# Performance work log

Hardware: AMD Instinct MI355X
Metric: run time of the kernel (lower is better)

The kernel has to match this reference:

```python
import jax, jax.numpy as jnp
import numpy as np

B, S, N, P = 16, 1, 6, 70000
H0, W0, DS = 448, 800, 4
H, W = H0 // DS, W0 // DS          # 112, 200
BEV_SIDE = 200


def _apply_4x4(RT, xyz):
    # RT: [M,4,4], xyz: [M,P,3] -> [M,P,3]
    xyz1 = jnp.concatenate([xyz, jnp.ones_like(xyz[..., :1])], axis=-1)
    return jnp.einsum('mij,mpj->mpi', RT, xyz1)[..., :3]


def _scale_intrinsics4(K, sx, sy):
    # K: [M,3,3] pinhole intrinsics -> scaled, embedded in 4x4
    M = K.shape[0]
    K4 = jnp.tile(jnp.eye(4, dtype=K.dtype), (M, 1, 1))
    K4 = K4.at[:, 0, 0].set(K[:, 0, 0] * sx)
    K4 = K4.at[:, 1, 1].set(K[:, 1, 1] * sy)
    K4 = K4.at[:, 0, 2].set(K[:, 0, 2] * sx)
    K4 = K4.at[:, 1, 2].set(K[:, 1, 2] * sy)
    return K4


def setup_inputs() -> dict:
    rng = np.random.default_rng(0)
    pts = rng.uniform(-50.0, 50.0, size=(B, 1, 1, P, 3)).astype(np.float32)
    pts[..., 2] = rng.uniform(-2.0, 4.0, size=(B, 1, 1, P)).astype(np.float32)
    ilu = rng.uniform(0.0, 255.0, size=(B, 1, 1, P, 1)).astype(np.float32)
    pcloud = np.concatenate([pts, ilu], axis=-1)
    # extrinsics: cam-to-car pose, 6 cameras at yaw 0..300deg
    E = np.tile(np.eye(4, dtype=np.float32), (B, S, N, 1, 1))
    for n in range(N):
        a = 2.0 * np.pi * n / N
        c, s = np.cos(a), np.sin(a)
        E[:, :, n, :3, :3] = np.array([[c, -s, 0], [s, c, 0], [0, 0, 1]], np.float32)
        E[:, :, n, :3, 3] = np.array([2.0 * c, 2.0 * s, 1.5], np.float32)
    K = np.tile(np.eye(3, dtype=np.float32), (B, S, N, 1, 1))
    K[..., 0, 0] = 500.0
    K[..., 1, 1] = 500.0
    K[..., 0, 2] = W0 / 2.0
    K[..., 1, 2] = H0 / 2.0
    V = np.tile(np.eye(4, dtype=np.float32), (B, 1, 1, 1, 1))
    V[..., 0, 0] = 2.0
    V[..., 1, 1] = 2.0
    V[..., 0, 3] = 100.0
    V[..., 1, 3] = 100.0
    return {
        'pcloud': jnp.asarray(pcloud),
        'extrinsics': jnp.asarray(E),
        'intrinsics': jnp.asarray(K),
        'view': jnp.asarray(V),
        'bev_side': BEV_SIDE,
    }


def reference(pcloud, extrinsics, intrinsics, view, bev_side):
    sx = sy = 1.0 / DS
    bsn = B * S * N
    lidar_coords = pcloud[:, 0, 0, :, :3]                      # [B,P,3]
    ilu = jnp.repeat(pcloud[:, 0, 0, :, 3], N, axis=0)         # [BSN,P]
    view2 = view[:, 0, 0]                                      # [B,4,4]
    lidar_view = _apply_4x4(jnp.linalg.inv(view2), lidar_coords)
    xyz_car = jnp.repeat(lidar_view, N, axis=0)                # [BSN,P,3]
    K = intrinsics.reshape(bsn, 3, 3)
    E = extrinsics.reshape(bsn, 4, 4)
    Rt = jnp.swapaxes(E[:, :3, :3], 1, 2)
    Einv = E.at[:, :3, :3].set(Rt).at[:, :3, 3:4].set(-jnp.matmul(Rt, E[:, :3, 3:4]))
    pixel_from_car = jnp.matmul(_scale_intrinsics4(K, sx, sy), Einv)
    z = _apply_4x4(Einv, xyz_car)[:, :, 2]                     # cam-frame depth
    xyz_pixel = _apply_4x4(pixel_from_car, xyz_car)            # [BSN,P,3]
    normalizer = xyz_pixel[:, :, 2]
    xy = xyz_pixel[:, :, :2] / jnp.maximum(normalizer[..., None], 1e-6)
    x_, y_ = xy[:, :, 0], xy[:, :, 1]
    valid = ((x_ > -0.5) & (x_ < W - 0.5) & (y_ > -0.5) & (y_ < H - 0.5) & (z > 0.0)).astype(pcloud.dtype)
    depth = jnp.clip(normalizer, 0.0, bev_side / 2 - 1) * valid
    vilu = jnp.clip(ilu * valid, 0.0, 255.0)
    ym = jnp.clip(y_, 0.0, H - 1).astype(jnp.int32)
    xm = jnp.clip(x_, 0.0, W - 1).astype(jnp.int32)
    b = jnp.broadcast_to(jnp.arange(bsn)[:, None], (bsn, P))
    depth_grid = jnp.zeros((bsn, H, W), pcloud.dtype).at[b, ym, xm].set(depth)
    ilu_grid = jnp.zeros((bsn, H, W), pcloud.dtype).at[b, ym, xm].set(vilu)
    ilu_grid = jnp.log1p(ilu_grid) / np.log(256.0)
    depth_grid = depth_grid / (bev_side / 2)
    return jnp.concatenate([depth_grid[:, None], ilu_grid[:, None]], axis=1)  # [BSN,2,H,W]
```

## Files before the change

kernel.cpp:

```cpp
#include <hip/hip_runtime.h>
#include <math.h>

#define B_    16
#define N_    6
#define P_    70000
#define H_    112
#define W_    200
#define HW_   (H_ * W_)
#define BSN_  (B_ * N_)
#define HALF_ 56
#define CELLS_ (HALF_ * W_)
#define THREADS_ 1024


__device__ __forceinline__ float rdot(const float r[4], float x, float y, float z) {
    float s = r[0] * x;
    s = fmaf(r[1], y, s);
    s = fmaf(r[2], z, s);
    s = s + r[3];
    return s;
}

__device__ __forceinline__ void inv4(const float* m, float* o) {
    float inv[16];
    inv[0]  =  m[5]*m[10]*m[15] - m[5]*m[11]*m[14] - m[9]*m[6]*m[15] + m[9]*m[7]*m[14] + m[13]*m[6]*m[11] - m[13]*m[7]*m[10];
    inv[4]  = -m[4]*m[10]*m[15] + m[4]*m[11]*m[14] + m[8]*m[6]*m[15] - m[8]*m[7]*m[14] - m[12]*m[6]*m[11] + m[12]*m[7]*m[10];
    inv[8]  =  m[4]*m[9]*m[15]  - m[4]*m[11]*m[13] - m[8]*m[5]*m[15] + m[8]*m[7]*m[13] + m[12]*m[5]*m[11] - m[12]*m[7]*m[9];
    inv[12] = -m[4]*m[9]*m[14]  + m[4]*m[10]*m[13] + m[8]*m[5]*m[14] - m[8]*m[6]*m[13] - m[12]*m[5]*m[10] + m[12]*m[6]*m[9];
    inv[1]  = -m[1]*m[10]*m[15] + m[1]*m[11]*m[14] + m[9]*m[2]*m[15] - m[9]*m[3]*m[14] - m[13]*m[2]*m[11] + m[13]*m[3]*m[10];
    inv[5]  =  m[0]*m[10]*m[15] - m[0]*m[11]*m[14] - m[8]*m[2]*m[15] + m[8]*m[3]*m[14] + m[12]*m[2]*m[11] - m[12]*m[3]*m[10];
    inv[9]  = -m[0]*m[9]*m[15]  + m[0]*m[11]*m[13] + m[8]*m[1]*m[15] - m[8]*m[3]*m[13] - m[12]*m[1]*m[11] + m[12]*m[3]*m[9];
    inv[13] =  m[0]*m[9]*m[14]  - m[0]*m[10]*m[13] - m[8]*m[1]*m[14] + m[8]*m[2]*m[13] + m[12]*m[1]*m[10] - m[12]*m[2]*m[9];
    inv[2]  =  m[1]*m[6]*m[15]  - m[1]*m[7]*m[14]  - m[5]*m[2]*m[15] + m[5]*m[3]*m[14] + m[13]*m[2]*m[7]  - m[13]*m[3]*m[6];
    inv[6]  = -m[0]*m[6]*m[15]  + m[0]*m[7]*m[14]  + m[4]*m[2]*m[15] - m[4]*m[3]*m[14] - m[12]*m[2]*m[7]  + m[12]*m[3]*m[6];
    inv[10] =  m[0]*m[5]*m[15]  - m[0]*m[7]*m[13]  - m[4]*m[1]*m[15] + m[4]*m[3]*m[13] + m[12]*m[1]*m[7]  - m[12]*m[3]*m[5];
    inv[14] = -m[0]*m[5]*m[14]  + m[0]*m[6]*m[13]  + m[4]*m[1]*m[14] - m[4]*m[2]*m[13] - m[12]*m[1]*m[6]  + m[12]*m[2]*m[5];
    inv[3]  = -m[1]*m[6]*m[11]  + m[1]*m[7]*m[10]  + m[5]*m[2]*m[11] - m[5]*m[3]*m[10] - m[9]*m[2]*m[7]   + m[9]*m[3]*m[6];
    inv[7]  =  m[0]*m[6]*m[11]  - m[0]*m[7]*m[10]  - m[4]*m[2]*m[11] + m[4]*m[3]*m[10] + m[8]*m[2]*m[7]   - m[8]*m[3]*m[6];
    inv[11] = -m[0]*m[5]*m[11]  + m[0]*m[7]*m[9]   + m[4]*m[1]*m[11] - m[4]*m[3]*m[9]  - m[8]*m[1]*m[7]   + m[8]*m[3]*m[5];
    inv[15] =  m[0]*m[5]*m[10]  - m[0]*m[6]*m[9]   - m[4]*m[1]*m[10] + m[4]*m[2]*m[9]  + m[8]*m[1]*m[6]   - m[8]*m[2]*m[5];
    float det = m[0]*inv[0] + m[1]*inv[4] + m[2]*inv[8] + m[3]*inv[12];
    float rdet = 1.0f / det;
    for (int i = 0; i < 16; ++i) o[i] = inv[i] * rdet;
}

__device__ __forceinline__ void cam_mats(const float* Ein, const float* Kin,
                                         float E2[4], float PFC[3][4]) {
    float Einv[4][4];
    for (int i = 0; i < 3; ++i)
        for (int j = 0; j < 3; ++j)
            Einv[i][j] = Ein[j * 4 + i];
    for (int i = 0; i < 3; ++i) {
        float s = Ein[0 * 4 + i] * Ein[0 * 4 + 3];
        s = fmaf(Ein[1 * 4 + i], Ein[1 * 4 + 3], s);
        s = fmaf(Ein[2 * 4 + i], Ein[2 * 4 + 3], s);
        Einv[i][3] = -s;
    }
    Einv[3][0] = Ein[12]; Einv[3][1] = Ein[13];
    Einv[3][2] = Ein[14]; Einv[3][3] = Ein[15];

    float K4[4][4] = {};
    K4[0][0] = Kin[0] * 0.25f;  K4[0][2] = Kin[2] * 0.25f;
    K4[1][1] = Kin[4] * 0.25f;  K4[1][2] = Kin[5] * 0.25f;
    K4[2][2] = 1.0f;            K4[3][3] = 1.0f;

    for (int i = 0; i < 3; ++i)
        for (int j = 0; j < 4; ++j) {
            float s = K4[i][0] * Einv[0][j];
            s = fmaf(K4[i][1], Einv[1][j], s);
            s = fmaf(K4[i][2], Einv[2][j], s);
            s = fmaf(K4[i][3], Einv[3][j], s);
            PFC[i][j] = s;
        }
    for (int j = 0; j < 4; ++j) E2[j] = Einv[2][j];
}


__global__ __launch_bounds__(THREADS_) void k_lidar_fused(
        const float4* __restrict__ pc, const float* __restrict__ extr,
        const float* __restrict__ intr, const float* __restrict__ view,
        float* __restrict__ out, const int* __restrict__ bev_side_p) {
    __shared__ int   win[CELLS_];
    __shared__ float sV[4][4];
    __shared__ float sE2[4];
    __shared__ float sP[3][4];

    const int i    = blockIdx.x;
    const int xcd  = i & 7;
    const int s    = i >> 3;
    const int b    = xcd + 8 * (s >= 12 ? 1 : 0);
    const int c12  = s % 12;
    const int m    = b * N_ + (c12 >> 1);
    const int rlo  = (c12 & 1) * HALF_;
    const int t    = threadIdx.x;

    if (t == 0) {
        float Vi[16];
        inv4(&view[b * 16], Vi);
        for (int ii = 0; ii < 4; ++ii)
            for (int j = 0; j < 4; ++j) sV[ii][j] = Vi[ii * 4 + j];
    } else if (t == 64) {
        float E2[4], PFC[3][4];
        cam_mats(&extr[m * 16], &intr[m * 9], E2, PFC);
        for (int j = 0; j < 4; ++j) sE2[j] = E2[j];
        for (int ii = 0; ii < 3; ++ii)
            for (int j = 0; j < 4; ++j) sP[ii][j] = PFC[ii][j];
    }
    for (int k = t; k < CELLS_; k += THREADS_) win[k] = -1;
    __syncthreads();

    const float4* pcb = pc + (size_t)b * P_;
    int c0 = -1, c1 = -1, c2 = -1, c3 = -1;
    for (int p = t; p < P_; p += THREADS_) {
        float4 pt = pcb[p];
        float lx = rdot(sV[0], pt.x, pt.y, pt.z);
        float ly = rdot(sV[1], pt.x, pt.y, pt.z);
        float lz = rdot(sV[2], pt.x, pt.y, pt.z);
        float px = rdot(sP[0], lx, ly, lz);
        float py = rdot(sP[1], lx, ly, lz);
        float pz = rdot(sP[2], lx, ly, lz);
        float denom = fmaxf(pz, 1e-6f);
        float x_ = px / denom;
        float y_ = py / denom;
        int ym = (int)fminf(fmaxf(y_, 0.0f), (float)(H_ - 1));
        int xm = (int)fminf(fmaxf(x_, 0.0f), (float)(W_ - 1));
        bool is_c = (xm == 0 || xm == W_ - 1) && (ym == 0 || ym == H_ - 1);
        int code = ((ym != 0) << 1) | (xm != 0);
        c0 = (is_c && code == 0) ? p : c0;
        c1 = (is_c && code == 1) ? p : c1;
        c2 = (is_c && code == 2) ? p : c2;
        c3 = (is_c && code == 3) ? p : c3;
        int rr = ym - rlo;
        if (!is_c && (unsigned)rr < (unsigned)HALF_)
            atomicMax(&win[rr * W_ + xm], p);
    }
    for (int d = 32; d; d >>= 1) {
        c0 = max(c0, __shfl_xor(c0, d));
        c1 = max(c1, __shfl_xor(c1, d));
        c2 = max(c2, __shfl_xor(c2, d));
        c3 = max(c3, __shfl_xor(c3, d));
    }
    if ((t & 63) == 0) {
        if (rlo == 0) {
            if (c0 >= 0) atomicMax(&win[0 * W_ + 0],        c0);
            if (c1 >= 0) atomicMax(&win[0 * W_ + (W_ - 1)], c1);
        } else {
            if (c2 >= 0) atomicMax(&win[(H_ - 1 - rlo) * W_ + 0],        c2);
            if (c3 >= 0) atomicMax(&win[(H_ - 1 - rlo) * W_ + (W_ - 1)], c3);
        }
    }
    __syncthreads();

    const float bev_half = (float)bev_side_p[0] * 0.5f;
    const float clip_hi  = bev_half - 1.0f;
    const int base0 = (m * 2) * HW_ + rlo * W_;
    for (int r = t; r < CELLS_; r += THREADS_) {
        int w = win[r];
        float depth = 0.0f, iluv = 0.0f;
        if (w >= 0) {
            float4 pt = pcb[w];
            float lx = rdot(sV[0], pt.x, pt.y, pt.z);
            float ly = rdot(sV[1], pt.x, pt.y, pt.z);
            float lz = rdot(sV[2], pt.x, pt.y, pt.z);
            float z  = rdot(sE2,   lx, ly, lz);
            float px = rdot(sP[0], lx, ly, lz);
            float py = rdot(sP[1], lx, ly, lz);
            float pz = rdot(sP[2], lx, ly, lz);
            float denom = fmaxf(pz, 1e-6f);
            float x_ = px / denom;
            float y_ = py / denom;
            bool valid = (x_ > -0.5f) && (x_ < (float)W_ - 0.5f) &&
                         (y_ > -0.5f) && (y_ < (float)H_ - 0.5f) && (z > 0.0f);
            if (valid) {
                float d = fminf(fmaxf(pz, 0.0f), clip_hi);
                depth = d / bev_half;
                float vi = fminf(fmaxf(pt.w, 0.0f), 255.0f);
                iluv = log1pf(vi) / 5.545177444479562f;
            }
        }
        out[base0 + r]       = depth;
        out[base0 + HW_ + r] = iluv;
    }
}


extern "C" void kernel_launch(void* const* d_in, const int* in_sizes, int n_in,
                              void* d_out, int out_size, void* d_ws, size_t ws_size,
                              hipStream_t stream) {
    const float4* pc  = (const float4*)d_in[0];
    const float* extr = (const float*)d_in[1];
    const float* intr = (const float*)d_in[2];
    const float* view = (const float*)d_in[3];
    const int*   bev  = (const int*)d_in[4];
    float* out = (float*)d_out;

    k_lidar_fused<<<dim3(BSN_ * 2), dim3(THREADS_), 0, stream>>>(
        pc, extr, intr, view, out, bev);
}
```

Before: 48.98 us.

## Precompute view-inverse transform in separate pass into workspace

```diff
diff --git a/kernel.cpp b/kernel.cpp
--- a/kernel.cpp
+++ b/kernel.cpp
@@ -19,6 +19,14 @@
     s = fmaf(r[2], z, s);
     s = s + r[3];
     return s;
+}
+
+__device__ __forceinline__ float rdot4(float r0, float r1, float r2, float r3,
+                                       float x, float y, float z) {
+    float s = r0 * x;
+    s = fmaf(r1, y, s);
+    s = fmaf(r2, z, s);
+    return s + r3;
 }
 
 __device__ __forceinline__ void inv4(const float* m, float* o) {
@@ -73,6 +81,137 @@
             PFC[i][j] = s;
         }
     for (int j = 0; j < 4; ++j) E2[j] = Einv[2][j];
+}
+
+
+#define K1_THREADS 256
+#define K1_SPLIT   64
+#define K1_CHUNK   1094
+
+__global__ __launch_bounds__(K1_THREADS) void k_pretransform(
+        const float4* __restrict__ pc, const float* __restrict__ view,
+        float4* __restrict__ tp) {
+    __shared__ float sV[3][4];
+    const int b = blockIdx.x;
+    if (threadIdx.x == 0) {
+        float Vi[16];
+        inv4(&view[b * 16], Vi);
+        for (int i = 0; i < 3; ++i)
+            for (int j = 0; j < 4; ++j) sV[i][j] = Vi[i * 4 + j];
+    }
+    __syncthreads();
+    const int start = blockIdx.y * K1_CHUNK;
+    const int end   = min(start + K1_CHUNK, P_);
+    const float4* pcb = pc + (size_t)b * P_;
+    float4* tpb = tp + (size_t)b * P_;
+    for (int p = start + threadIdx.x; p < end; p += K1_THREADS) {
+        float4 pt = pcb[p];
+        float lx = rdot(sV[0], pt.x, pt.y, pt.z);
+        float ly = rdot(sV[1], pt.x, pt.y, pt.z);
+        float lz = rdot(sV[2], pt.x, pt.y, pt.z);
+        tpb[p] = make_float4(lx, ly, lz, pt.w);
+    }
+}
+
+
+__global__ __launch_bounds__(THREADS_) void k_lidar_fused_ws(
+        const float4* __restrict__ tp, const float* __restrict__ extr,
+        const float* __restrict__ intr,
+        float* __restrict__ out, const int* __restrict__ bev_side_p) {
+    __shared__ int   win[CELLS_];
+    __shared__ float sE2[4];
+    __shared__ float sP[3][4];
+
+    const int i    = blockIdx.x;
+    const int xcd  = i & 7;
+    const int s    = i >> 3;
+    const int b    = xcd + 8 * (s >= 12 ? 1 : 0);
+    const int c12  = s % 12;
+    const int m    = b * N_ + (c12 >> 1);
+    const int rlo  = (c12 & 1) * HALF_;
+    const int t    = threadIdx.x;
+
+    if (t == 0) {
+        float E2[4], PFC[3][4];
+        cam_mats(&extr[m * 16], &intr[m * 9], E2, PFC);
+        for (int j = 0; j < 4; ++j) sE2[j] = E2[j];
+        for (int ii = 0; ii < 3; ++ii)
+            for (int j = 0; j < 4; ++j) sP[ii][j] = PFC[ii][j];
+    }
+    for (int k = t; k < CELLS_; k += THREADS_) win[k] = -1;
+    __syncthreads();
+
+    const float P00 = sP[0][0], P01 = sP[0][1], P02 = sP[0][2], P03 = sP[0][3];
+    const float P10 = sP[1][0], P11 = sP[1][1], P12 = sP[1][2], P13 = sP[1][3];
+    const float P20 = sP[2][0], P21 = sP[2][1], P22 = sP[2][2], P23 = sP[2][3];
+
+    const float4* tpb = tp + (size_t)b * P_;
+    int c0 = -1, c1 = -1, c2 = -1, c3 = -1;
+    for (int p = t; p < P_; p += THREADS_) {
+        float4 pt = tpb[p];
+        float px = rdot4(P00, P01, P02, P03, pt.x, pt.y, pt.z);
+        float py = rdot4(P10, P11, P12, P13, pt.x, pt.y, pt.z);
+        float pz = rdot4(P20, P21, P22, P23, pt.x, pt.y, pt.z);
+        float denom = fmaxf(pz, 1e-6f);
+        float x_ = px / denom;
+        float y_ = py / denom;
+        int ym = (int)fminf(fmaxf(y_, 0.0f), (float)(H_ - 1));
+        int xm = (int)fminf(fmaxf(x_, 0.0f), (float)(W_ - 1));
+        bool is_c = (xm == 0 || xm == W_ - 1) && (ym == 0 || ym == H_ - 1);
+        int code = ((ym != 0) << 1) | (xm != 0);
+        c0 = (is_c && code == 0) ? p : c0;
+        c1 = (is_c && code == 1) ? p : c1;
+        c2 = (is_c && code == 2) ? p : c2;
+        c3 = (is_c && code == 3) ? p : c3;
+        int rr = ym - rlo;
+        if (!is_c && (unsigned)rr < (unsigned)HALF_)
+            atomicMax(&win[rr * W_ + xm], p);
+    }
+    for (int d = 32; d; d >>= 1) {
+        c0 = max(c0, __shfl_xor(c0, d));
+        c1 = max(c1, __shfl_xor(c1, d));
+        c2 = max(c2, __shfl_xor(c2, d));
+        c3 = max(c3, __shfl_xor(c3, d));
+    }
+    if ((t & 63) == 0) {
+        if (rlo == 0) {
+            if (c0 >= 0) atomicMax(&win[0 * W_ + 0],        c0);
+            if (c1 >= 0) atomicMax(&win[0 * W_ + (W_ - 1)], c1);
+        } else {
+            if (c2 >= 0) atomicMax(&win[(H_ - 1 - rlo) * W_ + 0],        c2);
+            if (c3 >= 0) atomicMax(&win[(H_ - 1 - rlo) * W_ + (W_ - 1)], c3);
+        }
+    }
+    __syncthreads();
+
+    const float bev_half = (float)bev_side_p[0] * 0.5f;
+    const float clip_hi  = bev_half - 1.0f;
+    const float E20 = sE2[0], E21 = sE2[1], E22 = sE2[2], E23 = sE2[3];
+    const int base0 = (m * 2) * HW_ + rlo * W_;
+    for (int r = t; r < CELLS_; r += THREADS_) {
+        int w = win[r];
+        float depth = 0.0f, iluv = 0.0f;
+        if (w >= 0) {
+            float4 pt = tpb[w];
+            float z  = rdot4(E20, E21, E22, E23, pt.x, pt.y, pt.z);
+            float px = rdot4(P00, P01, P02, P03, pt.x, pt.y, pt.z);
+            float py = rdot4(P10, P11, P12, P13, pt.x, pt.y, pt.z);
+            float pz = rdot4(P20, P21, P22, P23, pt.x, pt.y, pt.z);
+            float denom = fmaxf(pz, 1e-6f);
+            float x_ = px / denom;
+            float y_ = py / denom;
+            bool valid = (x_ > -0.5f) && (x_ < (float)W_ - 0.5f) &&
+                         (y_ > -0.5f) && (y_ < (float)H_ - 0.5f) && (z > 0.0f);
+            if (valid) {
+                float d = fminf(fmaxf(pz, 0.0f), clip_hi);
+                depth = d / bev_half;
+                float vi = fminf(fmaxf(pt.w, 0.0f), 255.0f);
+                iluv = log1pf(vi) / 5.545177444479562f;
+            }
+        }
+        out[base0 + r]       = depth;
+        out[base0 + HW_ + r] = iluv;
+    }
 }
 
 
@@ -194,6 +333,14 @@
     const int*   bev  = (const int*)d_in[4];
     float* out = (float*)d_out;
 
-    k_lidar_fused<<<dim3(BSN_ * 2), dim3(THREADS_), 0, stream>>>(
-        pc, extr, intr, view, out, bev);
-}
+    const size_t need = (size_t)B_ * P_ * sizeof(float4);
+    if (ws_size >= need) {
+        float4* tp = (float4*)d_ws;
+        k_pretransform<<<dim3(B_, K1_SPLIT), dim3(K1_THREADS), 0, stream>>>(pc, view, tp);
+        k_lidar_fused_ws<<<dim3(BSN_ * 2), dim3(THREADS_), 0, stream>>>(
+            tp, extr, intr, out, bev);
+    } else {
+        k_lidar_fused<<<dim3(BSN_ * 2), dim3(THREADS_), 0, stream>>>(
+            pc, extr, intr, view, out, bev);
+    }
+}
```

Result: slower. 55.82 us (+14.0%).

## Split fused kernel into projection-code pass and quarter-tile scatter pass

Applied to the files above, without the earlier changes.

```diff
diff --git a/kernel.cpp b/kernel.cpp
--- a/kernel.cpp
+++ b/kernel.cpp
@@ -8,17 +8,36 @@
 #define W_    200
 #define HW_   (H_ * W_)
 #define BSN_  (B_ * N_)
-#define HALF_ 56
-#define CELLS_ (HALF_ * W_)
+#define QROWS  28
+#define QCELLS (QROWS * W_)
+#define NQ     4
 #define THREADS_ 1024
+
+#define WS_VINV 0
+#define WS_PFC  192
+#define WS_E2   1344
+#define WS_CODES_OFF 8192
+#define WS_NEED (WS_CODES_OFF + (size_t)BSN_ * P_ * 2)
+
+#define CC0 0u
+#define CC1 199u
+#define CC2 28416u
+#define CC3 28615u
 
 
 __device__ __forceinline__ float rdot(const float r[4], float x, float y, float z) {
     float s = r[0] * x;
     s = fmaf(r[1], y, s);
     s = fmaf(r[2], z, s);
-    s = s + r[3];
-    return s;
+    return s + r[3];
+}
+
+__device__ __forceinline__ float rdot4(float r0, float r1, float r2, float r3,
+                                       float x, float y, float z) {
+    float s = r0 * x;
+    s = fmaf(r1, y, s);
+    s = fmaf(r2, z, s);
+    return s + r3;
 }
 
 __device__ __forceinline__ void inv4(const float* m, float* o) {
@@ -76,6 +95,156 @@
 }
 
 
+__global__ __launch_bounds__(128) void k_mats(
+        const float* __restrict__ extr, const float* __restrict__ intr,
+        const float* __restrict__ view, float* __restrict__ wsf) {
+    const int t = threadIdx.x;
+    if (t < BSN_) {
+        float E2[4], PFC[3][4];
+        cam_mats(&extr[t * 16], &intr[t * 9], E2, PFC);
+        for (int i = 0; i < 3; ++i)
+            for (int j = 0; j < 4; ++j) wsf[WS_PFC + t * 12 + i * 4 + j] = PFC[i][j];
+        for (int j = 0; j < 4; ++j) wsf[WS_E2 + t * 4 + j] = E2[j];
+    } else if (t < BSN_ + B_) {
+        int b = t - BSN_;
+        float Vi[16];
+        inv4(&view[b * 16], Vi);
+        for (int k = 0; k < 12; ++k) wsf[WS_VINV + b * 12 + k] = Vi[k];
+    }
+}
+
+
+#define K1T 256
+
+__global__ __launch_bounds__(K1T) void k_codes(
+        const float4* __restrict__ pc, const float* __restrict__ wsf,
+        unsigned short* __restrict__ codes) {
+    __shared__ float sM[84];
+    const int b = blockIdx.x;
+    const int t = threadIdx.x;
+    if (t < 12)       sM[t] = wsf[WS_VINV + b * 12 + t];
+    else if (t < 84)  sM[t] = wsf[WS_PFC + b * 6 * 12 + (t - 12)];
+    __syncthreads();
+
+    float V[12], Pm[6][12];
+    #pragma unroll
+    for (int k = 0; k < 12; ++k) V[k] = sM[k];
+    #pragma unroll
+    for (int n = 0; n < 6; ++n)
+        #pragma unroll
+        for (int k = 0; k < 12; ++k) Pm[n][k] = sM[12 + n * 12 + k];
+
+    const int p = blockIdx.y * K1T + t;
+    if (p >= P_) return;
+    float4 pt = pc[(size_t)b * P_ + p];
+    float lx = rdot4(V[0], V[1], V[2],  V[3],  pt.x, pt.y, pt.z);
+    float ly = rdot4(V[4], V[5], V[6],  V[7],  pt.x, pt.y, pt.z);
+    float lz = rdot4(V[8], V[9], V[10], V[11], pt.x, pt.y, pt.z);
+    #pragma unroll
+    for (int n = 0; n < 6; ++n) {
+        float px = rdot4(Pm[n][0], Pm[n][1], Pm[n][2],  Pm[n][3],  lx, ly, lz);
+        float py = rdot4(Pm[n][4], Pm[n][5], Pm[n][6],  Pm[n][7],  lx, ly, lz);
+        float pz = rdot4(Pm[n][8], Pm[n][9], Pm[n][10], Pm[n][11], lx, ly, lz);
+        float denom = fmaxf(pz, 1e-6f);
+        float x_ = px / denom;
+        float y_ = py / denom;
+        int ym = (int)fminf(fmaxf(y_, 0.0f), (float)(H_ - 1));
+        int xm = (int)fminf(fmaxf(x_, 0.0f), (float)(W_ - 1));
+        codes[(size_t)(b * N_ + n) * P_ + p] = (unsigned short)((ym << 8) | xm);
+    }
+}
+
+
+__global__ __launch_bounds__(THREADS_) void k_scatfin(
+        const float4* __restrict__ pc, const unsigned short* __restrict__ codes,
+        const float* __restrict__ wsf, float* __restrict__ out,
+        const int* __restrict__ bev_side_p) {
+    __shared__ int   win[QCELLS];
+    __shared__ float sM[28];
+
+    const int i   = blockIdx.x;
+    const int xcd = i & 7;
+    const int j   = i >> 3;
+    const int b   = xcd + 8 * (j >= 24 ? 1 : 0);
+    const int r   = j % 24;
+    const int cam = r >> 2;
+    const int q   = r & 3;
+    const int m   = b * N_ + cam;
+    const int rlo = q * QROWS;
+    const int t   = threadIdx.x;
+
+    for (int k = t; k < QCELLS; k += THREADS_) win[k] = -1;
+    if (t < 12)       sM[t] = wsf[WS_VINV + b * 12 + t];
+    else if (t < 24)  sM[t] = wsf[WS_PFC + m * 12 + (t - 12)];
+    else if (t < 28)  sM[t] = wsf[WS_E2 + m * 4 + (t - 24)];
+    __syncthreads();
+
+    const unsigned short* cm = codes + (size_t)m * P_;
+    int c0 = -1, c1 = -1, c2 = -1, c3 = -1;
+    for (int p = t; p < P_; p += THREADS_) {
+        unsigned int c = cm[p];
+        bool i0 = (c == CC0), i1 = (c == CC1), i2 = (c == CC2), i3 = (c == CC3);
+        c0 = i0 ? p : c0;  c1 = i1 ? p : c1;
+        c2 = i2 ? p : c2;  c3 = i3 ? p : c3;
+        int ym = (int)(c >> 8), xm = (int)(c & 255u);
+        int rr = ym - rlo;
+        if (!(i0 | i1 | i2 | i3) && (unsigned)rr < (unsigned)QROWS)
+            atomicMax(&win[rr * W_ + xm], p);
+    }
+    for (int d = 32; d; d >>= 1) {
+        c0 = max(c0, __shfl_xor(c0, d));
+        c1 = max(c1, __shfl_xor(c1, d));
+        c2 = max(c2, __shfl_xor(c2, d));
+        c3 = max(c3, __shfl_xor(c3, d));
+    }
+    if ((t & 63) == 0) {
+        if (q == 0) {
+            if (c0 >= 0) atomicMax(&win[0],   c0);
+            if (c1 >= 0) atomicMax(&win[199], c1);
+        } else if (q == 3) {
+            if (c2 >= 0) atomicMax(&win[(H_ - 1 - rlo) * W_ + 0],   c2);
+            if (c3 >= 0) atomicMax(&win[(H_ - 1 - rlo) * W_ + 199], c3);
+        }
+    }
+    __syncthreads();
+
+    const float bev_half = (float)bev_side_p[0] * 0.5f;
+    const float clip_hi  = bev_half - 1.0f;
+    const float4* pcb = pc + (size_t)b * P_;
+    const int base0 = (m * 2) * HW_ + rlo * W_;
+    for (int rr = t; rr < QCELLS; rr += THREADS_) {
+        int w = win[rr];
+        float depth = 0.0f, iluv = 0.0f;
+        if (w >= 0) {
+            float4 pt = pcb[w];
+            float lx = rdot4(sM[0],  sM[1],  sM[2],  sM[3],  pt.x, pt.y, pt.z);
+            float ly = rdot4(sM[4],  sM[5],  sM[6],  sM[7],  pt.x, pt.y, pt.z);
+            float lz = rdot4(sM[8],  sM[9],  sM[10], sM[11], pt.x, pt.y, pt.z);
+            float z  = rdot4(sM[24], sM[25], sM[26], sM[27], lx, ly, lz);
+            float px = rdot4(sM[12], sM[13], sM[14], sM[15], lx, ly, lz);
+            float py = rdot4(sM[16], sM[17], sM[18], sM[19], lx, ly, lz);
+            float pz = rdot4(sM[20], sM[21], sM[22], sM[23], lx, ly, lz);
+            float denom = fmaxf(pz, 1e-6f);
+            float x_ = px / denom;
+            float y_ = py / denom;
+            bool valid = (x_ > -0.5f) && (x_ < (float)W_ - 0.5f) &&
+                         (y_ > -0.5f) && (y_ < (float)H_ - 0.5f) && (z > 0.0f);
+            if (valid) {
+                float d = fminf(fmaxf(pz, 0.0f), clip_hi);
+                depth = d / bev_half;
+                float vi = fminf(fmaxf(pt.w, 0.0f), 255.0f);
+                iluv = log1pf(vi) / 5.545177444479562f;
+            }
+        }
+        out[base0 + rr]       = depth;
+        out[base0 + HW_ + rr] = iluv;
+    }
+}
+
+
+#define HALF_ 56
+#define CELLS_ (HALF_ * W_)
+
 __global__ __launch_bounds__(THREADS_) void k_lidar_fused(
         const float4* __restrict__ pc, const float* __restrict__ extr,
         const float* __restrict__ intr, const float* __restrict__ view,
@@ -98,13 +267,13 @@
         float Vi[16];
         inv4(&view[b * 16], Vi);
         for (int ii = 0; ii < 4; ++ii)
-            for (int j = 0; j < 4; ++j) sV[ii][j] = Vi[ii * 4 + j];
+            for (int jj = 0; jj < 4; ++jj) sV[ii][jj] = Vi[ii * 4 + jj];
     } else if (t == 64) {
         float E2[4], PFC[3][4];
         cam_mats(&extr[m * 16], &intr[m * 9], E2, PFC);
-        for (int j = 0; j < 4; ++j) sE2[j] = E2[j];
+        for (int jj = 0; jj < 4; ++jj) sE2[jj] = E2[jj];
         for (int ii = 0; ii < 3; ++ii)
-            for (int j = 0; j < 4; ++j) sP[ii][j] = PFC[ii][j];
+            for (int jj = 0; jj < 4; ++jj) sP[ii][jj] = PFC[ii][jj];
     }
     for (int k = t; k < CELLS_; k += THREADS_) win[k] = -1;
     __syncthreads();
@@ -142,11 +311,11 @@
     }
     if ((t & 63) == 0) {
         if (rlo == 0) {
-            if (c0 >= 0) atomicMax(&win[0 * W_ + 0],        c0);
-            if (c1 >= 0) atomicMax(&win[0 * W_ + (W_ - 1)], c1);
+            if (c0 >= 0) atomicMax(&win[0],   c0);
+            if (c1 >= 0) atomicMax(&win[199], c1);
         } else {
-            if (c2 >= 0) atomicMax(&win[(H_ - 1 - rlo) * W_ + 0],        c2);
-            if (c3 >= 0) atomicMax(&win[(H_ - 1 - rlo) * W_ + (W_ - 1)], c3);
+            if (c2 >= 0) atomicMax(&win[(H_ - 1 - rlo) * W_ + 0],   c2);
+            if (c3 >= 0) atomicMax(&win[(H_ - 1 - rlo) * W_ + 199], c3);
         }
     }
     __syncthreads();
@@ -154,8 +323,8 @@
     const float bev_half = (float)bev_side_p[0] * 0.5f;
     const float clip_hi  = bev_half - 1.0f;
     const int base0 = (m * 2) * HW_ + rlo * W_;
-    for (int r = t; r < CELLS_; r += THREADS_) {
-        int w = win[r];
+    for (int rr = t; rr < CELLS_; rr += THREADS_) {
+        int w = win[rr];
         float depth = 0.0f, iluv = 0.0f;
         if (w >= 0) {
             float4 pt = pcb[w];
@@ -178,8 +347,8 @@
                 iluv = log1pf(vi) / 5.545177444479562f;
             }
         }
-        out[base0 + r]       = depth;
-        out[base0 + HW_ + r] = iluv;
+        out[base0 + rr]       = depth;
+        out[base0 + HW_ + rr] = iluv;
     }
 }
 
@@ -194,6 +363,14 @@
     const int*   bev  = (const int*)d_in[4];
     float* out = (float*)d_out;
 
-    k_lidar_fused<<<dim3(BSN_ * 2), dim3(THREADS_), 0, stream>>>(
-        pc, extr, intr, view, out, bev);
-}
+    if (ws_size >= WS_NEED) {
+        float* wsf = (float*)d_ws;
+        unsigned short* codes = (unsigned short*)((char*)d_ws + WS_CODES_OFF);
+        k_mats<<<dim3(1), dim3(128), 0, stream>>>(extr, intr, view, wsf);
+        k_codes<<<dim3(B_, (P_ + K1T - 1) / K1T), dim3(K1T), 0, stream>>>(pc, wsf, codes);
+        k_scatfin<<<dim3(BSN_ * NQ), dim3(THREADS_), 0, stream>>>(pc, codes, wsf, out, bev);
+    } else {
+        k_lidar_fused<<<dim3(BSN_ * 2), dim3(THREADS_), 0, stream>>>(
+            pc, extr, intr, view, out, bev);
+    }
+}
```

New measurement: 55.73 us. 13.8% more time.
